# Kernel optimization log

Hardware: AMD Instinct MI355X
Metric: run time of the kernel (lower is better)

The kernel has to match this reference:

```python
import jax, jax.numpy as jnp
import numpy as np

TEMPERATURE = 8.0  # sqrt(d_head=64)
NEG_INF = -1e15


def setup_inputs() -> dict:
    key = jax.random.key(0)
    k1, k2_, k3, k4, k5, k6 = jax.random.split(key, 6)
    BH, N, D = 16, 2048, 64
    B = 2  # edge batch; BH // B == 8 heads
    return {
        "q": jax.random.normal(k1, (BH, N, D), dtype=jnp.float32),
        "k": jax.random.normal(k2_, (BH, N, D), dtype=jnp.float32),
        "v": jax.random.normal(k3, (BH, N, D), dtype=jnp.float32),
        "k2": jax.random.normal(k4, (BH, N, D), dtype=jnp.float32),
        "mask": jax.random.randint(k5, (BH, 1, N), 0, 2) > 0,
        "edge": jax.random.randint(k6, (B, N, N), 0, 2).astype(jnp.int32),
    }


def reference(q, k, v, k2, mask, edge):
    # attn scores: [bh, n, m]
    attn = jnp.einsum("bnd,bmd->bnm", q, k) / TEMPERATURE
    # torch .repeat along dim0 == tile
    reps = attn.shape[0] // edge.shape[0]
    edge_t = jnp.tile(edge, (reps, 1, 1))
    attn = jnp.where(edge_t == 0, NEG_INF, attn)
    attn = jnp.where(mask, NEG_INF, attn)
    attn = jax.nn.softmax(attn, axis=2)  # dropout p=0 (eval)
    output = jnp.einsum("bnm,bmd->bnd", attn, v)
    # non_linear=False, so no sigmoid
    return (output, attn)
```

## Files before the change

### kernel.cpp

```cpp
#include <hip/hip_runtime.h>
#include <stdint.h>
#include <math.h>

#define BH_ 16
#define N_  2048
#define D_  64
#define NEGV (-1e15f)

typedef __attribute__((ext_vector_type(8))) short bf16x8;
typedef __attribute__((ext_vector_type(8))) unsigned short us8;
typedef __attribute__((ext_vector_type(4))) float f32x4;

#define OFF_MASKU8 0u
#define OFF_MBITS  32768u
#define OFF_EBITS  65536u
#define OFF_QBF    1114112u
#define OFF_KBF    5308416u
#define OFF_VT     9502720u
#define WS_NEEDED  13697024u

__device__ __forceinline__ unsigned short f2bf(float f) {
    unsigned u = __float_as_uint(f);
    return (unsigned short)((u + 0x7FFFu + ((u >> 16) & 1u)) >> 16);
}

__global__ __launch_bounds__(256)
void prep_all(const float* __restrict__ q, const float* __restrict__ k,
              const float* __restrict__ v, const void* __restrict__ mraw,
              const int* __restrict__ edge,
              unsigned short* __restrict__ qbf, unsigned short* __restrict__ kbf,
              unsigned short* __restrict__ vT,
              unsigned short* __restrict__ e16, unsigned long long* __restrict__ mbits)
{
    __shared__ unsigned short shbuf[64][72];
    __shared__ int flag;
    const int bid = blockIdx.x;
    const int t   = threadIdx.x;

    if (bid < 2048) {
        const int idx = bid * 256 + t;
        const int4* p = (const int4*)(edge + (size_t)idx * 16);
        unsigned m = 0;
        #pragma unroll
        for (int i = 0; i < 4; ++i) {
            const int4 vv = p[i];
            m |= (vv.x != 0 ? 1u : 0u) << (i * 4 + 0);
            m |= (vv.y != 0 ? 1u : 0u) << (i * 4 + 1);
            m |= (vv.z != 0 ? 1u : 0u) << (i * 4 + 2);
            m |= (vv.w != 0 ? 1u : 0u) << (i * 4 + 3);
        }
        e16[idx] = (unsigned short)m;
    } else if (bid < 2560) {
        const int b2 = bid - 2048;
        const int rt = b2 & 31, bh = b2 >> 5;
        const size_t base = ((size_t)bh * N_ + (size_t)rt * 64) * D_;
        #pragma unroll
        for (int i = 0; i < 4; ++i) {
            const int idx = t + i * 256;
            float4 f = *(const float4*)(q + base + (size_t)idx * 4);
            ushort4 s; s.x = f2bf(f.x); s.y = f2bf(f.y); s.z = f2bf(f.z); s.w = f2bf(f.w);
            *(ushort4*)(qbf + base + (size_t)idx * 4) = s;
            f = *(const float4*)(k + base + (size_t)idx * 4);
            s.x = f2bf(f.x); s.y = f2bf(f.y); s.z = f2bf(f.z); s.w = f2bf(f.w);
            *(ushort4*)(kbf + base + (size_t)idx * 4) = s;
            f = *(const float4*)(v + base + (size_t)idx * 4);
            const int row = idx >> 4;
            const int d0  = (idx & 15) * 4;
            shbuf[d0 + 0][row] = f2bf(f.x);
            shbuf[d0 + 1][row] = f2bf(f.y);
            shbuf[d0 + 2][row] = f2bf(f.z);
            shbuf[d0 + 3][row] = f2bf(f.w);
        }
        __syncthreads();
        const int d  = t >> 2;
        const int c4 = (t & 3) * 16;
        const size_t ob = ((size_t)bh * D_ + d) * N_ + (size_t)rt * 64 + c4;
        *(us8*)(vT + ob)     = *(us8*)&shbuf[d][c4];
        *(us8*)(vT + ob + 8) = *(us8*)&shbuf[d][c4 + 8];
    } else {
        const int bh = bid - 2560;
        if (t == 0) flag = 0;
        __syncthreads();
        const int* mi = (const int*)mraw;
        int bad = 0;
        for (int i = t; i < 8192; i += 256)
            if ((unsigned)mi[i] > 1u) bad = 1;
        if (bad) atomicOr(&flag, 1);
        __syncthreads();
        const int is_u8 = flag;
        const uint8_t* m8 = (const uint8_t*)mraw;
        const int w4 = t >> 6, l = t & 63;
        for (int it = 0; it < 8; ++it) {
            const int pos = bh * 2048 + it * 256 + w4 * 64 + l;
            const bool on = is_u8 ? (m8[pos] != 0) : (mi[pos] != 0);
            unsigned long long bal = __ballot(on);
            if (l == 0) mbits[bh * 32 + it * 4 + w4] = bal;
        }
    }
}

__global__ __launch_bounds__(256)
void attn_v3(const unsigned short* __restrict__ qbf,
             const unsigned short* __restrict__ kbf,
             const unsigned short* __restrict__ vT,
             const unsigned long long* __restrict__ ebits,
             const unsigned long long* __restrict__ mbits,
             float* __restrict__ out, float* __restrict__ attn)
{
    __shared__ unsigned short kls[4][4096];
    __shared__ unsigned short vls[4][4096];
    __shared__ char  pbuf[4][2048];
    __shared__ float lsum[4][16];

    const int tile = blockIdx.x;
    const int bh   = blockIdx.y;
    const int t    = threadIdx.x;
    const int w    = t >> 6;
    const int lane = t & 63;
    const int l15  = lane & 15;
    const int lg   = lane >> 4;
    const int l8   = lane & 7;
    const int lrow = lane >> 3;
    const int rbase = tile * 16;

    const unsigned short* qb = qbf + (size_t)bh * N_ * D_;
    const unsigned short* kb = kbf + (size_t)bh * N_ * D_;
    const unsigned short* vb = vT  + (size_t)bh * D_ * N_;
    const unsigned long long* ebrow =
        ebits + ((size_t)(bh & 1) * N_ + (size_t)(rbase + l15)) * 32;
    const unsigned long long* mb = mbits + bh * 32;
    float* outb = out + (size_t)bh * N_ * D_;
    float* arow = attn + (size_t)bh * N_ * N_ + (size_t)(rbase + l15) * N_ + lg * 4;

    const bf16x8 aq0 = *(const bf16x8*)(qb + (size_t)(rbase + l15) * D_ + lg * 8);
    const bf16x8 aq1 = *(const bf16x8*)(qb + (size_t)(rbase + l15) * D_ + lg * 8 + 32);

    unsigned short* myk = kls[w];
    unsigned short* myv = vls[w];
    const int sb = lrow * 64 + ((l8 ^ lrow) * 8);

    float lacc = 0.f;
    {
        const unsigned short* src = kb + (size_t)w * 4096;
        us8 rk[8];
        #pragma unroll
        for (int j = 0; j < 8; ++j) rk[j] = *(const us8*)(src + j * 512 + lane * 8);
        #pragma unroll
        for (int j = 0; j < 8; ++j) *(us8*)(myk + j * 512 + sb) = rk[j];
    }
    #pragma unroll 1
    for (int i = 0; i < 8; ++i) {
        const int kc = i * 4 + w;
        us8 nk[8];
        if (i < 7) {
            const unsigned short* src = kb + (size_t)(kc + 4) * 4096;
            #pragma unroll
            for (int j = 0; j < 8; ++j) nk[j] = *(const us8*)(src + j * 512 + lane * 8);
        }
        const unsigned long long wbits = ebrow[kc] & ~mb[kc];
        #pragma unroll
        for (int nt = 0; nt < 4; ++nt) {
            const int row = nt * 16 + l15, sw = row & 7;
            const bf16x8 k0 = *(const bf16x8*)(myk + row * 64 + ((lg ^ sw) * 8));
            const bf16x8 k1 = *(const bf16x8*)(myk + row * 64 + (((lg + 4) ^ sw) * 8));
            f32x4 c = (f32x4){0.f, 0.f, 0.f, 0.f};
            c = __builtin_amdgcn_mfma_f32_16x16x32_bf16(k0, aq0, c, 0, 0, 0);
            c = __builtin_amdgcn_mfma_f32_16x16x32_bf16(k1, aq1, c, 0, 0, 0);
            const unsigned bits = (unsigned)(wbits >> (nt * 16 + lg * 4)) & 0xFu;
            #pragma unroll
            for (int r = 0; r < 4; ++r)
                lacc += ((bits >> r) & 1u) ? __expf(c[r] * 0.125f) : 0.f;
        }
        if (i < 7) {
            #pragma unroll
            for (int j = 0; j < 8; ++j) *(us8*)(myk + j * 512 + sb) = nk[j];
        }
    }
    lacc += __shfl_xor(lacc, 16);
    lacc += __shfl_xor(lacc, 32);
    lsum[w][l15] = lacc;
    __syncthreads();
    const float inv = 1.0f / (lsum[0][l15] + lsum[1][l15] + lsum[2][l15] + lsum[3][l15]);

    f32x4 o[4];
    #pragma unroll
    for (int nt = 0; nt < 4; ++nt) o[nt] = (f32x4){0.f, 0.f, 0.f, 0.f};

    char* pbc = pbuf[w];
    const int swzP = (l15 & 7) << 4;
    const int ab0 = (l15 * 128 + lg * 16)      ^ swzP;
    const int ab1 = (l15 * 128 + lg * 16 + 64) ^ swzP;
    const int gvb = lrow * 2048 + l8 * 8;

    {
        const unsigned short* src = kb + (size_t)w * 4096;
        const unsigned short* srv = vb + (size_t)w * 64;
        us8 rk[8];
        #pragma unroll
        for (int j = 0; j < 8; ++j) rk[j] = *(const us8*)(src + j * 512 + lane * 8);
        #pragma unroll
        for (int j = 0; j < 8; ++j) *(us8*)(myk + j * 512 + sb) = rk[j];
        #pragma unroll
        for (int j = 0; j < 8; ++j) rk[j] = *(const us8*)(srv + j * 16384 + gvb);
        #pragma unroll
        for (int j = 0; j < 8; ++j) *(us8*)(myv + j * 512 + sb) = rk[j];
    }
    #pragma unroll 1
    for (int i = 0; i < 8; ++i) {
        const int kc = i * 4 + w;
        us8 nk[8];
        if (i < 7) {
            const unsigned short* src = kb + (size_t)(kc + 4) * 4096;
            #pragma unroll
            for (int j = 0; j < 8; ++j) nk[j] = *(const us8*)(src + j * 512 + lane * 8);
        }
        const unsigned long long wbits = ebrow[kc] & ~mb[kc];
        float* astore = arow + kc * 64;
        #pragma unroll
        for (int nt = 0; nt < 4; ++nt) {
            const int row = nt * 16 + l15, sw = row & 7;
            const bf16x8 k0 = *(const bf16x8*)(myk + row * 64 + ((lg ^ sw) * 8));
            const bf16x8 k1 = *(const bf16x8*)(myk + row * 64 + (((lg + 4) ^ sw) * 8));
            f32x4 c = (f32x4){0.f, 0.f, 0.f, 0.f};
            c = __builtin_amdgcn_mfma_f32_16x16x32_bf16(k0, aq0, c, 0, 0, 0);
            c = __builtin_amdgcn_mfma_f32_16x16x32_bf16(k1, aq1, c, 0, 0, 0);
            const unsigned bits = (unsigned)(wbits >> (nt * 16 + lg * 4)) & 0xFu;
            float4 e;
            e.x = (bits & 1u) ? __expf(c[0] * 0.125f) * inv : 0.f;
            e.y = (bits & 2u) ? __expf(c[1] * 0.125f) * inv : 0.f;
            e.z = (bits & 4u) ? __expf(c[2] * 0.125f) * inv : 0.f;
            e.w = (bits & 8u) ? __expf(c[3] * 0.125f) * inv : 0.f;
            *(float4*)(astore + nt * 16) = e;
            ushort4 pe;
            pe.x = f2bf(e.x); pe.y = f2bf(e.y); pe.z = f2bf(e.z); pe.w = f2bf(e.w);
            const int wbyte = (l15 * 128 + nt * 32 + lg * 8) ^ swzP;
            *(ushort4*)(pbc + wbyte) = pe;
        }
        if (i < 7) {
            #pragma unroll
            for (int j = 0; j < 8; ++j) *(us8*)(myk + j * 512 + sb) = nk[j];
        }
        us8 nv[8];
        if (i < 7) {
            const unsigned short* srv = vb + (size_t)(kc + 4) * 64;
            #pragma unroll
            for (int j = 0; j < 8; ++j) nv[j] = *(const us8*)(srv + j * 16384 + gvb);
        }
        const bf16x8 ap0 = *(const bf16x8*)(pbc + ab0);
        const bf16x8 ap1 = *(const bf16x8*)(pbc + ab1);
        #pragma unroll
        for (int nt = 0; nt < 4; ++nt) {
            const int row = nt * 16 + l15, sw = row & 7;
            const bf16x8 bv0 = *(const bf16x8*)(myv + row * 64 + ((lg ^ sw) * 8));
            const bf16x8 bv1 = *(const bf16x8*)(myv + row * 64 + (((lg + 4) ^ sw) * 8));
            o[nt] = __builtin_amdgcn_mfma_f32_16x16x32_bf16(ap0, bv0, o[nt], 0, 0, 0);
            o[nt] = __builtin_amdgcn_mfma_f32_16x16x32_bf16(ap1, bv1, o[nt], 0, 0, 0);
        }
        if (i < 7) {
            #pragma unroll
            for (int j = 0; j < 8; ++j) *(us8*)(myv + j * 512 + sb) = nv[j];
        }
    }

    __syncthreads();
    float* lred = (float*)kls;
    #pragma unroll
    for (int nt = 0; nt < 4; ++nt)
        #pragma unroll
        for (int r = 0; r < 4; ++r)
            lred[(size_t)w * 1088 + (lg * 4 + r) * 68 + nt * 16 + l15] = o[nt][r];
    __syncthreads();
    for (int oi = t; oi < 1024; oi += 256) {
        const int row = oi >> 6, d = oi & 63;
        const float s = lred[row * 68 + d] + lred[1088 + row * 68 + d]
                      + lred[2176 + row * 68 + d] + lred[3264 + row * 68 + d];
        outb[(size_t)(rbase + row) * D_ + d] = s;
    }
}

__global__ __launch_bounds__(256)
void normalize_mask(const void* __restrict__ mask_raw, uint8_t* __restrict__ mask_out)
{
    __shared__ int is_u8;
    const int t = threadIdx.x;
    if (t == 0) is_u8 = 0;
    __syncthreads();
    const int* mi = (const int*)mask_raw;
    int bad = 0;
    for (int i = t; i < 8192; i += 256)
        if ((unsigned)mi[i] > 1u) bad = 1;
    if (bad) atomicOr(&is_u8, 1);
    __syncthreads();
    const int total = BH_ * N_;
    if (is_u8) {
        const uint8_t* m8 = (const uint8_t*)mask_raw;
        for (int i = t; i < total; i += 256) mask_out[i] = m8[i] ? 1 : 0;
    } else {
        for (int i = t; i < total; i += 256) mask_out[i] = (uint8_t)mi[i];
    }
}

__global__ __launch_bounds__(256)
void attn_fused(const float* __restrict__ q, const float* __restrict__ k,
                const float* __restrict__ v, const uint8_t* __restrict__ mask,
                const int* __restrict__ edge, float* __restrict__ out,
                float* __restrict__ attn)
{
    __shared__ float qsT[D_][64 + 4];
    __shared__ float kt [D_][64 + 4];
    __shared__ float vs [64][D_ + 4];
    const int tile = blockIdx.x, bh = blockIdx.y, t = threadIdx.x;
    const int rg = t >> 4, cg = t & 15, r0 = rg * 4, c0 = cg * 4;
    const int row_base = tile * 64;
    const float* qb = q + (size_t)bh * N_ * D_;
    const float* kb = k + (size_t)bh * N_ * D_;
    const float* vb = v + (size_t)bh * N_ * D_;
    const uint8_t* mbp = mask + (size_t)bh * N_;
    const int* ebp = edge + (size_t)(bh & 1) * N_ * N_;
    float* outb = out + (size_t)bh * N_ * D_;
    float* attnb = attn + (size_t)bh * N_ * N_;
    {
        const int rr = t >> 2, dblk = (t & 3) * 16;
        const float* src = qb + (size_t)(row_base + rr) * D_ + dblk;
        #pragma unroll
        for (int qq = 0; qq < 4; ++qq) {
            float4 val = *(const float4*)(src + qq * 4);
            qsT[dblk + qq*4 + 0][rr] = val.x; qsT[dblk + qq*4 + 1][rr] = val.y;
            qsT[dblk + qq*4 + 2][rr] = val.z; qsT[dblk + qq*4 + 3][rr] = val.w;
        }
    }
    float m_i[4], l_i[4];
    #pragma unroll
    for (int i = 0; i < 4; ++i) { m_i[i] = -INFINITY; l_i[i] = 0.f; }
    for (int kc = 0; kc < 32; ++kc) {
        __syncthreads();
        {
            const int ccr = t >> 2, dblk = (t & 3) * 16;
            const float* src = kb + (size_t)(kc * 64 + ccr) * D_ + dblk;
            #pragma unroll
            for (int qq = 0; qq < 4; ++qq) {
                float4 val = *(const float4*)(src + qq * 4);
                kt[dblk + qq*4 + 0][ccr] = val.x; kt[dblk + qq*4 + 1][ccr] = val.y;
                kt[dblk + qq*4 + 2][ccr] = val.z; kt[dblk + qq*4 + 3][ccr] = val.w;
            }
        }
        __syncthreads();
        float sc[4][4];
        #pragma unroll
        for (int i = 0; i < 4; ++i) { sc[i][0]=sc[i][1]=sc[i][2]=sc[i][3]=0.f; }
        for (int d = 0; d < D_; ++d) {
            const float4 qv = *(const float4*)&qsT[d][r0];
            const float4 kv = *(const float4*)&kt[d][c0];
            #pragma unroll
            for (int i = 0; i < 4; ++i) {
                const float qi = (i==0)?qv.x:(i==1)?qv.y:(i==2)?qv.z:qv.w;
                sc[i][0] = fmaf(qi, kv.x, sc[i][0]); sc[i][1] = fmaf(qi, kv.y, sc[i][1]);
                sc[i][2] = fmaf(qi, kv.z, sc[i][2]); sc[i][3] = fmaf(qi, kv.w, sc[i][3]);
            }
        }
        const int cbase = kc * 64 + c0;
        const uint8_t m0 = mbp[cbase], m1 = mbp[cbase+1], m2 = mbp[cbase+2], m3 = mbp[cbase+3];
        #pragma unroll
        for (int i = 0; i < 4; ++i) {
            const int rglob = row_base + r0 + i;
            const int4 e4 = *(const int4*)(ebp + (size_t)rglob * N_ + cbase);
            float s0 = sc[i][0]*0.125f, s1 = sc[i][1]*0.125f, s2 = sc[i][2]*0.125f, s3 = sc[i][3]*0.125f;
            if (e4.x == 0 || m0) s0 = NEGV; if (e4.y == 0 || m1) s1 = NEGV;
            if (e4.z == 0 || m2) s2 = NEGV; if (e4.w == 0 || m3) s3 = NEGV;
            float cmax = fmaxf(fmaxf(s0,s1), fmaxf(s2,s3));
            cmax = fmaxf(cmax, __shfl_xor(cmax,1)); cmax = fmaxf(cmax, __shfl_xor(cmax,2));
            cmax = fmaxf(cmax, __shfl_xor(cmax,4)); cmax = fmaxf(cmax, __shfl_xor(cmax,8));
            const float nm = fmaxf(m_i[i], cmax);
            float ss = __expf(s0-nm)+__expf(s1-nm)+__expf(s2-nm)+__expf(s3-nm);
            ss += __shfl_xor(ss,1); ss += __shfl_xor(ss,2); ss += __shfl_xor(ss,4); ss += __shfl_xor(ss,8);
            l_i[i] = l_i[i]*__expf(m_i[i]-nm) + ss; m_i[i] = nm;
        }
    }
    float inv_l[4];
    #pragma unroll
    for (int i = 0; i < 4; ++i) inv_l[i] = 1.0f / l_i[i];
    float oacc[4][4];
    #pragma unroll
    for (int i = 0; i < 4; ++i) { oacc[i][0]=oacc[i][1]=oacc[i][2]=oacc[i][3]=0.f; }
    for (int kc = 0; kc < 32; ++kc) {
        __syncthreads();
        {
            const int ccr = t >> 2, dblk = (t & 3) * 16;
            const float* src = kb + (size_t)(kc * 64 + ccr) * D_ + dblk;
            #pragma unroll
            for (int qq = 0; qq < 4; ++qq) {
                float4 val = *(const float4*)(src + qq * 4);
                kt[dblk + qq*4 + 0][ccr] = val.x; kt[dblk + qq*4 + 1][ccr] = val.y;
                kt[dblk + qq*4 + 2][ccr] = val.z; kt[dblk + qq*4 + 3][ccr] = val.w;
            }
            const float* srcv = vb + (size_t)(kc * 64 + ccr) * D_ + dblk;
            #pragma unroll
            for (int qq = 0; qq < 4; ++qq)
                *(float4*)&vs[ccr][dblk + qq * 4] = *(const float4*)(srcv + qq * 4);
        }
        __syncthreads();
        float sc[4][4];
        #pragma unroll
        for (int i = 0; i < 4; ++i) { sc[i][0]=sc[i][1]=sc[i][2]=sc[i][3]=0.f; }
        for (int d = 0; d < D_; ++d) {
            const float4 qv = *(const float4*)&qsT[d][r0];
            const float4 kv = *(const float4*)&kt[d][c0];
            #pragma unroll
            for (int i = 0; i < 4; ++i) {
                const float qi = (i==0)?qv.x:(i==1)?qv.y:(i==2)?qv.z:qv.w;
                sc[i][0] = fmaf(qi, kv.x, sc[i][0]); sc[i][1] = fmaf(qi, kv.y, sc[i][1]);
                sc[i][2] = fmaf(qi, kv.z, sc[i][2]); sc[i][3] = fmaf(qi, kv.w, sc[i][3]);
            }
        }
        const int cbase = kc * 64 + c0;
        const uint8_t m0 = mbp[cbase], m1 = mbp[cbase+1], m2 = mbp[cbase+2], m3 = mbp[cbase+3];
        float p[4][4];
        #pragma unroll
        for (int i = 0; i < 4; ++i) {
            const int rglob = row_base + r0 + i;
            const int4 e4 = *(const int4*)(ebp + (size_t)rglob * N_ + cbase);
            float s0 = sc[i][0]*0.125f, s1 = sc[i][1]*0.125f, s2 = sc[i][2]*0.125f, s3 = sc[i][3]*0.125f;
            if (e4.x == 0 || m0) s0 = NEGV; if (e4.y == 0 || m1) s1 = NEGV;
            if (e4.z == 0 || m2) s2 = NEGV; if (e4.w == 0 || m3) s3 = NEGV;
            p[i][0] = __expf(s0-m_i[i])*inv_l[i]; p[i][1] = __expf(s1-m_i[i])*inv_l[i];
            p[i][2] = __expf(s2-m_i[i])*inv_l[i]; p[i][3] = __expf(s3-m_i[i])*inv_l[i];
            *(float4*)&attnb[(size_t)rglob * N_ + cbase] = make_float4(p[i][0],p[i][1],p[i][2],p[i][3]);
        }
        __syncthreads();
        #pragma unroll
        for (int i = 0; i < 4; ++i)
            *(float4*)&kt[r0 + i][c0] = make_float4(p[i][0],p[i][1],p[i][2],p[i][3]);
        __syncthreads();
        for (int c4 = 0; c4 < 64; c4 += 4) {
            float prr[4][4];
            #pragma unroll
            for (int i = 0; i < 4; ++i) {
                const float4 tmp = *(const float4*)&kt[r0 + i][c4];
                prr[i][0]=tmp.x; prr[i][1]=tmp.y; prr[i][2]=tmp.z; prr[i][3]=tmp.w;
            }
            #pragma unroll
            for (int cc = 0; cc < 4; ++cc) {
                const float4 vv = *(const float4*)&vs[c4 + cc][c0];
                #pragma unroll
                for (int i = 0; i < 4; ++i) {
                    oacc[i][0] = fmaf(prr[i][cc], vv.x, oacc[i][0]);
                    oacc[i][1] = fmaf(prr[i][cc], vv.y, oacc[i][1]);
                    oacc[i][2] = fmaf(prr[i][cc], vv.z, oacc[i][2]);
                    oacc[i][3] = fmaf(prr[i][cc], vv.w, oacc[i][3]);
                }
            }
        }
    }
    #pragma unroll
    for (int i = 0; i < 4; ++i)
        *(float4*)&outb[(size_t)(row_base + r0 + i) * D_ + c0] =
            make_float4(oacc[i][0], oacc[i][1], oacc[i][2], oacc[i][3]);
}

extern "C" void kernel_launch(void* const* d_in, const int* in_sizes, int n_in,
                              void* d_out, int out_size, void* d_ws, size_t ws_size,
                              hipStream_t stream) {
    const float* q    = (const float*)d_in[0];
    const float* k    = (const float*)d_in[1];
    const float* v    = (const float*)d_in[2];
    const void*  mraw = d_in[4];
    const int*   edge = (const int*)d_in[5];

    float* out  = (float*)d_out;
    float* attn = (float*)d_out + (size_t)BH_ * N_ * D_;

    char* ws = (char*)d_ws;

    if (ws_size < (size_t)WS_NEEDED) {
        uint8_t* mask_u8 = (uint8_t*)(ws + OFF_MASKU8);
        normalize_mask<<<1, 256, 0, stream>>>(mraw, mask_u8);
        attn_fused<<<dim3(32, 16), 256, 0, stream>>>(q, k, v, mask_u8, edge, out, attn);
        return;
    }

    unsigned long long* mbits = (unsigned long long*)(ws + OFF_MBITS);
    unsigned short*     e16   = (unsigned short*)(ws + OFF_EBITS);
    unsigned short*     qbf   = (unsigned short*)(ws + OFF_QBF);
    unsigned short*     kbf   = (unsigned short*)(ws + OFF_KBF);
    unsigned short*     vT    = (unsigned short*)(ws + OFF_VT);

    prep_all<<<dim3(2576), 256, 0, stream>>>(q, k, v, mraw, edge,
                                             qbf, kbf, vT, e16, mbits);
    attn_v3<<<dim3(N_ / 16, BH_), 256, 0, stream>>>(
        qbf, kbf, vT, (const unsigned long long*)e16, mbits, out, attn);
}
```

Measured before the change: 148.4 us.

## Split PV output columns across warps with shared double-buffered K/V chunks

The second pass now has all four waves work on the same 64-key chunk. Each wave computes one 16-column slice of the scores and one 16-column slice of the output, sharing a single P buffer and a double-buffered K/V tile in LDS. This drops the cross-wave reduction of the output and the per-wave 8-row K/V staging, and cuts LDS use so more blocks can be resident. In exchange it adds two block-wide barriers per chunk across 32 iterations, which may limit latency hiding.

```diff
diff --git a/kernel.cpp b/kernel.cpp
--- a/kernel.cpp
+++ b/kernel.cpp
@@ -100,16 +100,15 @@
 }
 
 __global__ __launch_bounds__(256)
-void attn_v3(const unsigned short* __restrict__ qbf,
+void attn_v4(const unsigned short* __restrict__ qbf,
              const unsigned short* __restrict__ kbf,
              const unsigned short* __restrict__ vT,
              const unsigned long long* __restrict__ ebits,
              const unsigned long long* __restrict__ mbits,
              float* __restrict__ out, float* __restrict__ attn)
 {
-    __shared__ unsigned short kls[4][4096];
-    __shared__ unsigned short vls[4][4096];
-    __shared__ char  pbuf[4][2048];
+    __shared__ unsigned short sKV[4][4096];
+    __shared__ char  pbufS[2048];
     __shared__ float lsum[4][16];
 
     const int tile = blockIdx.x;
@@ -135,10 +134,8 @@
     const bf16x8 aq0 = *(const bf16x8*)(qb + (size_t)(rbase + l15) * D_ + lg * 8);
     const bf16x8 aq1 = *(const bf16x8*)(qb + (size_t)(rbase + l15) * D_ + lg * 8 + 32);
 
-    unsigned short* myk = kls[w];
-    unsigned short* myv = vls[w];
+    unsigned short* myk = sKV[w];
     const int sb = lrow * 64 + ((l8 ^ lrow) * 8);
-
     float lacc = 0.f;
     {
         const unsigned short* src = kb + (size_t)w * 4096;
@@ -182,100 +179,88 @@
     __syncthreads();
     const float inv = 1.0f / (lsum[0][l15] + lsum[1][l15] + lsum[2][l15] + lsum[3][l15]);
 
-    f32x4 o[4];
-    #pragma unroll
-    for (int nt = 0; nt < 4; ++nt) o[nt] = (f32x4){0.f, 0.f, 0.f, 0.f};
-
-    char* pbc = pbuf[w];
+    const int s0row = t >> 3;
+    const int s1row = s0row + 32;
+    const int t8    = t & 7;
+    const int ds0 = s0row * 64 + ((t8 ^ (s0row & 7)) * 8);
+    const int ds1 = s1row * 64 + ((t8 ^ (s1row & 7)) * 8);
+
+    {
+        const us8 a0 = *(const us8*)(kb + (size_t)t * 8);
+        const us8 a1 = *(const us8*)(kb + (size_t)(t + 256) * 8);
+        const us8 b0 = *(const us8*)(vb + (size_t)s0row * 2048 + t8 * 8);
+        const us8 b1 = *(const us8*)(vb + (size_t)s1row * 2048 + t8 * 8);
+        *(us8*)(sKV[0] + ds0) = a0;
+        *(us8*)(sKV[0] + ds1) = a1;
+        *(us8*)(sKV[2] + ds0) = b0;
+        *(us8*)(sKV[2] + ds1) = b1;
+        __syncthreads();
+    }
+
+    f32x4 o = (f32x4){0.f, 0.f, 0.f, 0.f};
     const int swzP = (l15 & 7) << 4;
     const int ab0 = (l15 * 128 + lg * 16)      ^ swzP;
     const int ab1 = (l15 * 128 + lg * 16 + 64) ^ swzP;
-    const int gvb = lrow * 2048 + l8 * 8;
-
-    {
-        const unsigned short* src = kb + (size_t)w * 4096;
-        const unsigned short* srv = vb + (size_t)w * 64;
-        us8 rk[8];
-        #pragma unroll
-        for (int j = 0; j < 8; ++j) rk[j] = *(const us8*)(src + j * 512 + lane * 8);
-        #pragma unroll
-        for (int j = 0; j < 8; ++j) *(us8*)(myk + j * 512 + sb) = rk[j];
-        #pragma unroll
-        for (int j = 0; j < 8; ++j) rk[j] = *(const us8*)(srv + j * 16384 + gvb);
-        #pragma unroll
-        for (int j = 0; j < 8; ++j) *(us8*)(myv + j * 512 + sb) = rk[j];
-    }
+    const int pwb = (l15 * 128 + w * 32 + lg * 8) ^ swzP;
+    const int rowq = w * 16 + l15;
+    const int swq  = l15 & 7;
+    const int koff0 = rowq * 64 + ((lg ^ swq) * 8);
+    const int koff1 = rowq * 64 + (((lg + 4) ^ swq) * 8);
+
     #pragma unroll 1
-    for (int i = 0; i < 8; ++i) {
-        const int kc = i * 4 + w;
-        us8 nk[8];
-        if (i < 7) {
-            const unsigned short* src = kb + (size_t)(kc + 4) * 4096;
-            #pragma unroll
-            for (int j = 0; j < 8; ++j) nk[j] = *(const us8*)(src + j * 512 + lane * 8);
-        }
+    for (int kc = 0; kc < 32; ++kc) {
+        const int cur = kc & 1;
+        us8 nk0, nk1, nv0, nv1;
+        if (kc < 31) {
+            const unsigned short* srck = kb + (size_t)(kc + 1) * 4096;
+            const unsigned short* srcv = vb + (size_t)(kc + 1) * 64;
+            nk0 = *(const us8*)(srck + (size_t)t * 8);
+            nk1 = *(const us8*)(srck + (size_t)(t + 256) * 8);
+            nv0 = *(const us8*)(srcv + (size_t)s0row * 2048 + t8 * 8);
+            nv1 = *(const us8*)(srcv + (size_t)s1row * 2048 + t8 * 8);
+        }
+        const unsigned short* kcur = sKV[cur];
+        const bf16x8 k0 = *(const bf16x8*)(kcur + koff0);
+        const bf16x8 k1 = *(const bf16x8*)(kcur + koff1);
+        f32x4 c = (f32x4){0.f, 0.f, 0.f, 0.f};
+        c = __builtin_amdgcn_mfma_f32_16x16x32_bf16(k0, aq0, c, 0, 0, 0);
+        c = __builtin_amdgcn_mfma_f32_16x16x32_bf16(k1, aq1, c, 0, 0, 0);
         const unsigned long long wbits = ebrow[kc] & ~mb[kc];
-        float* astore = arow + kc * 64;
-        #pragma unroll
-        for (int nt = 0; nt < 4; ++nt) {
-            const int row = nt * 16 + l15, sw = row & 7;
-            const bf16x8 k0 = *(const bf16x8*)(myk + row * 64 + ((lg ^ sw) * 8));
-            const bf16x8 k1 = *(const bf16x8*)(myk + row * 64 + (((lg + 4) ^ sw) * 8));
-            f32x4 c = (f32x4){0.f, 0.f, 0.f, 0.f};
-            c = __builtin_amdgcn_mfma_f32_16x16x32_bf16(k0, aq0, c, 0, 0, 0);
-            c = __builtin_amdgcn_mfma_f32_16x16x32_bf16(k1, aq1, c, 0, 0, 0);
-            const unsigned bits = (unsigned)(wbits >> (nt * 16 + lg * 4)) & 0xFu;
-            float4 e;
-            e.x = (bits & 1u) ? __expf(c[0] * 0.125f) * inv : 0.f;
-            e.y = (bits & 2u) ? __expf(c[1] * 0.125f) * inv : 0.f;
-            e.z = (bits & 4u) ? __expf(c[2] * 0.125f) * inv : 0.f;
-            e.w = (bits & 8u) ? __expf(c[3] * 0.125f) * inv : 0.f;
-            *(float4*)(astore + nt * 16) = e;
-            ushort4 pe;
-            pe.x = f2bf(e.x); pe.y = f2bf(e.y); pe.z = f2bf(e.z); pe.w = f2bf(e.w);
-            const int wbyte = (l15 * 128 + nt * 32 + lg * 8) ^ swzP;
-            *(ushort4*)(pbc + wbyte) = pe;
-        }
-        if (i < 7) {
-            #pragma unroll
-            for (int j = 0; j < 8; ++j) *(us8*)(myk + j * 512 + sb) = nk[j];
-        }
-        us8 nv[8];
-        if (i < 7) {
-            const unsigned short* srv = vb + (size_t)(kc + 4) * 64;
-            #pragma unroll
-            for (int j = 0; j < 8; ++j) nv[j] = *(const us8*)(srv + j * 16384 + gvb);
-        }
-        const bf16x8 ap0 = *(const bf16x8*)(pbc + ab0);
-        const bf16x8 ap1 = *(const bf16x8*)(pbc + ab1);
-        #pragma unroll
-        for (int nt = 0; nt < 4; ++nt) {
-            const int row = nt * 16 + l15, sw = row & 7;
-            const bf16x8 bv0 = *(const bf16x8*)(myv + row * 64 + ((lg ^ sw) * 8));
-            const bf16x8 bv1 = *(const bf16x8*)(myv + row * 64 + (((lg + 4) ^ sw) * 8));
-            o[nt] = __builtin_amdgcn_mfma_f32_16x16x32_bf16(ap0, bv0, o[nt], 0, 0, 0);
-            o[nt] = __builtin_amdgcn_mfma_f32_16x16x32_bf16(ap1, bv1, o[nt], 0, 0, 0);
-        }
-        if (i < 7) {
-            #pragma unroll
-            for (int j = 0; j < 8; ++j) *(us8*)(myv + j * 512 + sb) = nv[j];
-        }
-    }
-
-    __syncthreads();
-    float* lred = (float*)kls;
+        const unsigned bits = (unsigned)(wbits >> (w * 16 + lg * 4)) & 0xFu;
+        float4 e;
+        e.x = (bits & 1u) ? __expf(c[0] * 0.125f) * inv : 0.f;
+        e.y = (bits & 2u) ? __expf(c[1] * 0.125f) * inv : 0.f;
+        e.z = (bits & 4u) ? __expf(c[2] * 0.125f) * inv : 0.f;
+        e.w = (bits & 8u) ? __expf(c[3] * 0.125f) * inv : 0.f;
+        *(float4*)(arow + kc * 64 + w * 16) = e;
+        ushort4 pe;
+        pe.x = f2bf(e.x); pe.y = f2bf(e.y); pe.z = f2bf(e.z); pe.w = f2bf(e.w);
+        *(ushort4*)(pbufS + pwb) = pe;
+
+        __syncthreads();
+
+        const bf16x8 ap0 = *(const bf16x8*)(pbufS + ab0);
+        const bf16x8 ap1 = *(const bf16x8*)(pbufS + ab1);
+        const unsigned short* vcur = sKV[2 + cur];
+        const bf16x8 bv0 = *(const bf16x8*)(vcur + koff0);
+        const bf16x8 bv1 = *(const bf16x8*)(vcur + koff1);
+        o = __builtin_amdgcn_mfma_f32_16x16x32_bf16(ap0, bv0, o, 0, 0, 0);
+        o = __builtin_amdgcn_mfma_f32_16x16x32_bf16(ap1, bv1, o, 0, 0, 0);
+
+        if (kc < 31) {
+            unsigned short* kn = sKV[cur ^ 1];
+            unsigned short* vn = sKV[2 + (cur ^ 1)];
+            *(us8*)(kn + ds0) = nk0;
+            *(us8*)(kn + ds1) = nk1;
+            *(us8*)(vn + ds0) = nv0;
+            *(us8*)(vn + ds1) = nv1;
+        }
+        __syncthreads();
+    }
+
     #pragma unroll
-    for (int nt = 0; nt < 4; ++nt)
-        #pragma unroll
-        for (int r = 0; r < 4; ++r)
-            lred[(size_t)w * 1088 + (lg * 4 + r) * 68 + nt * 16 + l15] = o[nt][r];
-    __syncthreads();
-    for (int oi = t; oi < 1024; oi += 256) {
-        const int row = oi >> 6, d = oi & 63;
-        const float s = lred[row * 68 + d] + lred[1088 + row * 68 + d]
-                      + lred[2176 + row * 68 + d] + lred[3264 + row * 68 + d];
-        outb[(size_t)(rbase + row) * D_ + d] = s;
-    }
+    for (int r = 0; r < 4; ++r)
+        outb[(size_t)(rbase + lg * 4 + r) * D_ + w * 16 + l15] = o[r];
 }
 
 __global__ __launch_bounds__(256)
@@ -486,6 +471,6 @@
 
     prep_all<<<dim3(2576), 256, 0, stream>>>(q, k, v, mraw, edge,
                                              qbf, kbf, vT, e16, mbits);
-    attn_v3<<<dim3(N_ / 16, BH_), 256, 0, stream>>>(
+    attn_v4<<<dim3(N_ / 16, BH_), 256, 0, stream>>>(
         qbf, kbf, vT, (const unsigned long long*)e16, mbits, out, attn);
 }
```

New measurement: 152.7 us. 1.03x slower.
